# Kernel optimization log

Measured on AMD Instinct MI355X. Metric: run time of the kernel, lower is better.

## Reference

```python
import jax, jax.numpy as jnp
import numpy as np

N_NODES = 20000
N_EDGES = 320000
N_ADJ = 4
D = 256
CSTR = [0, 1]          # constrained adjacency subset for the last step
RATIO = 1.0
LN_EPS = 1e-5


def setup_inputs() -> dict:
    key = jax.random.key(0)
    ks = jax.random.split(key, 10)
    x = jax.random.normal(ks[0], (N_NODES, D), dtype=jnp.float32)
    rows = jax.random.randint(ks[1], (N_ADJ, N_EDGES), 0, N_NODES)
    cols = jax.random.randint(ks[2], (N_ADJ, N_EDGES), 0, N_NODES)
    vals = jax.random.uniform(ks[3], (N_ADJ, N_EDGES), dtype=jnp.float32)
    W = jax.random.normal(ks[4], (D, D), dtype=jnp.float32) * (1.0 / np.sqrt(D))
    b = jax.random.normal(ks[5], (D,), dtype=jnp.float32) * 0.02
    ws_seq_0 = jax.random.uniform(ks[6], (2, N_ADJ - 1), dtype=jnp.float32)
    ws_seq_1 = jax.random.uniform(ks[7], (len(CSTR),), dtype=jnp.float32)
    ws_res_0 = jax.random.uniform(ks[8], (1, N_ADJ), dtype=jnp.float32)
    ws_res_1 = jax.random.uniform(ks[9], (2, len(CSTR) + 1), dtype=jnp.float32)
    return {"x": x, "rows": rows, "cols": cols, "vals": vals, "W": W, "b": b,
            "ws_seq_0": ws_seq_0, "ws_seq_1": ws_seq_1,
            "ws_res_0": ws_res_0, "ws_res_1": ws_res_1}


def reference(x, rows, cols, vals, W, b, ws_seq_0, ws_seq_1, ws_res_0, ws_res_1):
    n_nodes = x.shape[0]

    def spmm(a, h):
        # sparse [n,n] @ h : gather source features, scale, scatter-add by row
        return jax.ops.segment_sum(vals[a][:, None] * h[cols[a]], rows[a],
                                   num_segments=n_nodes)

    def op(h, adj_ids, w):
        # Op with k=1: random.sample selects ALL operators -> weighted mean
        acc = w[0] * spmm(adj_ids[0], h)
        for j, a in enumerate(adj_ids[1:], start=1):
            acc = acc + w[j] * spmm(a, h)
        return acc / len(adj_ids)

    h = x @ W + b                      # affine: [n_nodes, D]
    states = [h]
    # step i=0: seq only (res sum over states[:0] is empty -> 0), edge == 1
    s1 = op(states[0], [0, 1, 2], ws_seq_0[0])          # adjs[:-1]
    states.append(s1)
    # step i=1: seq on states[1] over adjs[:-1], res on states[0] over all adjs
    s2 = op(states[1], [0, 1, 2], ws_seq_0[1]) + RATIO * op(states[0], [0, 1, 2, 3], ws_res_0[0])
    states.append(s2)
    # last step: cstr adjacencies for seq; cstr + last adj for residuals
    out_seq = op(states[2], CSTR, ws_seq_1)
    res_ids = CSTR + [N_ADJ - 1]
    out_res = op(states[0], res_ids, ws_res_1[0]) + op(states[1], res_ids, ws_res_1[1])
    out = out_seq + RATIO * out_res
    # LayerNorm without affine params
    mu = jnp.mean(out, axis=-1, keepdims=True)
    var = jnp.var(out, axis=-1, keepdims=True)
    out = (out - mu) * jax.lax.rsqrt(var + LN_EPS)
    return jax.nn.gelu(out, approximate=False)
```

## Files before the change

### kernel.cpp

```cpp
#include <hip/hip_runtime.h>
#include <hip/hip_bf16.h>

#define N_NODES 20000
#define N_EDGES 320000
#define N_ADJ   4
#define D       256
#define DH      128
#define RPA     20004

#define NBUCK   79
#define NGRP    40
#define EPB     8000
#define GCAP    192
#define NBSORT  (NBUCK * N_ADJ)
#define MMBLK   1250

typedef __attribute__((ext_vector_type(8))) short bf8;
typedef __attribute__((ext_vector_type(4))) float f4;


__device__ __forceinline__ unsigned f2bf_bits(float x) {
    unsigned u = __float_as_uint(x);
    return (u + 0x7FFFu + ((u >> 16) & 1u)) >> 16;
}
__device__ __forceinline__ unsigned pack_bf2(float lo, float hi) {
    return f2bf_bits(lo) | (f2bf_bits(hi) << 16);
}
__device__ __forceinline__ float bf_lo(unsigned p) { return __uint_as_float(p << 16); }
__device__ __forceinline__ float bf_hi(unsigned p) { return __uint_as_float(p & 0xFFFF0000u); }


__global__ __launch_bounds__(1024) void prep_kernel(const int* __restrict__ rows,
                                                    const int* __restrict__ cols,
                                                    const float* __restrict__ vals,
                                                    int* __restrict__ cnt,
                                                    uint2* __restrict__ stage,
                                                    const float* __restrict__ W,
                                                    uint4* __restrict__ wh,
                                                    uint4* __restrict__ wl) {
    __shared__ int lcnt[NBUCK];
    int g = blockIdx.x, a = blockIdx.y, t = threadIdx.x;

    if (g >= NGRP) {
        if (a != 0) return;
        for (int i = (g - NGRP) * 1024 + t; i < 8192; i += 2048) {
            int lane = i & 63;
            int tile = i >> 6;
            int ks = tile >> 4, n = tile & 15;
            int m = lane & 15, quad = lane >> 4;
            int col = n * 16 + m;
            int k0  = ks * 32 + quad * 8;
            unsigned hbits[8], lbits[8];
            #pragma unroll
            for (int j = 0; j < 8; ++j) {
                float v = W[(k0 + j) * D + col];
                unsigned hb = f2bf_bits(v);
                float lo = v - __uint_as_float(hb << 16);
                hbits[j] = hb;
                lbits[j] = f2bf_bits(lo);
            }
            uint4 hh, ll;
            hh.x = hbits[0] | (hbits[1] << 16); hh.y = hbits[2] | (hbits[3] << 16);
            hh.z = hbits[4] | (hbits[5] << 16); hh.w = hbits[6] | (hbits[7] << 16);
            ll.x = lbits[0] | (lbits[1] << 16); ll.y = lbits[2] | (lbits[3] << 16);
            ll.z = lbits[4] | (lbits[5] << 16); ll.w = lbits[6] | (lbits[7] << 16);
            wh[i] = hh;
            wl[i] = ll;
        }
        return;
    }

    if (t < NBUCK) lcnt[t] = 0;
    __syncthreads();
    int e0 = g * EPB;
    for (int i = 0; i < EPB; i += 1024) {
        int e = e0 + i + t;
        if (i + t < EPB) {
            int r   = rows[a * N_EDGES + e];
            int c   = cols[a * N_EDGES + e];
            float v = vals[a * N_EDGES + e];
            int b   = r >> 8;
            int idx = atomicAdd(&lcnt[b], 1);
            if (idx < GCAP) {
                stage[(size_t)((a * NBUCK + b) * NGRP + g) * GCAP + idx] =
                    make_uint2((f2bf_bits(v) << 16) | (unsigned)c, (unsigned)(r & 255));
            }
        }
    }
    __syncthreads();
    if (t < NBUCK) cnt[(a * NBUCK + t) * NGRP + g] = min(lcnt[t], GCAP);
}


__global__ __launch_bounds__(256) void bsmm_kernel(const float* __restrict__ x,
                                                   const uint4* __restrict__ wh,
                                                   const uint4* __restrict__ wl,
                                                   const float* __restrict__ bvec,
                                                   unsigned* __restrict__ hp,
                                                   const int* __restrict__ cnt,
                                                   const uint2* __restrict__ stage,
                                                   unsigned* __restrict__ csr,
                                                   int* __restrict__ row_ptr) {
    __shared__ int cbs[NGRP];
    __shared__ int scn[256];
    __shared__ int offs[256];
    __shared__ int gbase_s;
    int t = threadIdx.x;

    if (blockIdx.x >= NBSORT) {
        int wid = t >> 6, lane = t & 63;
        int r0 = (blockIdx.x - NBSORT) * 16;
        int m = lane & 15, quad = lane >> 4;

        const float* xr = x + (size_t)(r0 + m) * D + quad * 8;
        bf8 ah[8], al[8];
        #pragma unroll
        for (int ks = 0; ks < 8; ++ks) {
            float4 v0 = *(const float4*)(xr + ks * 32);
            float4 v1 = *(const float4*)(xr + ks * 32 + 4);
            float xs[8] = {v0.x, v0.y, v0.z, v0.w, v1.x, v1.y, v1.z, v1.w};
            #pragma unroll
            for (int j = 0; j < 8; ++j) {
                unsigned hb = f2bf_bits(xs[j]);
                float lo = xs[j] - __uint_as_float(hb << 16);
                ah[ks][j] = (short)hb;
                al[ks][j] = (short)f2bf_bits(lo);
            }
        }

        #pragma unroll
        for (int i = 0; i < 4; ++i) {
            int n = wid * 4 + i;
            f4 c = {0.f, 0.f, 0.f, 0.f};
            #pragma unroll
            for (int ks = 0; ks < 8; ++ks) {
                uint4 bh4 = wh[(ks * 16 + n) * 64 + lane];
                uint4 bl4 = wl[(ks * 16 + n) * 64 + lane];
                bf8 bh = *(bf8*)&bh4;
                bf8 bl = *(bf8*)&bl4;
                c = __builtin_amdgcn_mfma_f32_16x16x32_bf16(ah[ks], bh, c, 0, 0, 0);
                c = __builtin_amdgcn_mfma_f32_16x16x32_bf16(al[ks], bh, c, 0, 0, 0);
                c = __builtin_amdgcn_mfma_f32_16x16x32_bf16(ah[ks], bl, c, 0, 0, 0);
            }
            int col = n * 16 + m;
            float bb = bvec[col];
            #pragma unroll
            for (int reg = 0; reg < 4; ++reg) {
                float v = c[reg] + bb;
                float o = __shfl_xor(v, 1, 64);
                if ((m & 1) == 0) {
                    hp[(r0 + quad * 4 + reg) * DH + (col >> 1)] = pack_bf2(v, o);
                }
            }
        }
        return;
    }

    int linear = blockIdx.x;
    int a = linear / NBUCK, b = linear % NBUCK;

    if (t == 0) gbase_s = 0;
    scn[t] = 0;
    offs[t] = 0;
    if (t < NGRP) cbs[t] = cnt[(a * NBUCK + b) * NGRP + t];
    __syncthreads();

    int part = 0;
    for (int i = t; i < b * NGRP; i += 256) part += cnt[a * (NBUCK * NGRP) + i];
    #pragma unroll
    for (int off = 32; off > 0; off >>= 1) part += __shfl_xor(part, off, 64);
    if ((t & 63) == 0) atomicAdd(&gbase_s, part);

    const uint2* sb = stage + (size_t)(a * NBUCK + b) * NGRP * GCAP;

    for (int i = t; i < NGRP * GCAP; i += 256) {
        int g = i / GCAP, idx = i - g * GCAP;
        if (idx < cbs[g]) atomicAdd(&scn[sb[i].y], 1);
    }
    __syncthreads();

    int mycnt = scn[t];
    for (int off = 1; off < 256; off <<= 1) {
        int add = (t >= off) ? scn[t - off] : 0;
        __syncthreads();
        scn[t] += add;
        __syncthreads();
    }
    int excl = scn[t] - mycnt;
    __syncthreads();
    scn[t] = excl;
    __syncthreads();

    int gbase = gbase_s;
    for (int i = t; i < NGRP * GCAP; i += 256) {
        int g = i / GCAP, idx = i - g * GCAP;
        if (idx < cbs[g]) {
            uint2 rec = sb[i];
            int pos = scn[rec.y] + atomicAdd(&offs[rec.y], 1);
            csr[(size_t)a * N_EDGES + gbase + pos] = rec.x;
        }
    }
    int r = b * 256 + t;
    if (r <= N_NODES) row_ptr[(size_t)a * RPA + r] = gbase + excl;
}


__device__ __forceinline__ void gather_seg(const unsigned* __restrict__ E, int beg, int end,
                                           const uint2* __restrict__ feat2, int lane,
                                           float* __restrict__ s ) {
    int n = end - beg;
    const unsigned* e = E + beg;
    int m8 = n & ~7;
    if (m8) {
        unsigned rec[8];
        #pragma unroll
        for (int j = 0; j < 8; ++j) rec[j] = e[j];
        for (int i = 8; ; i += 8) {
            uint2 p[8];
            #pragma unroll
            for (int j = 0; j < 8; ++j)
                p[j] = feat2[((rec[j] & 0xFFFFu) << 6) + lane];
            bool more = i < m8;
            unsigned nrec[8];
            if (more) {
                #pragma unroll
                for (int j = 0; j < 8; ++j) nrec[j] = e[i + j];
            }
            #pragma unroll
            for (int j = 0; j < 8; ++j) {
                float v = __uint_as_float(rec[j] & 0xFFFF0000u);
                s[0] += v * bf_lo(p[j].x);
                s[1] += v * bf_hi(p[j].x);
                s[2] += v * bf_lo(p[j].y);
                s[3] += v * bf_hi(p[j].y);
            }
            if (!more) break;
            #pragma unroll
            for (int j = 0; j < 8; ++j) rec[j] = nrec[j];
        }
    }
    for (int i = m8; i < n; ++i) {
        unsigned rr = e[i];
        uint2 pp = feat2[((rr & 0xFFFFu) << 6) + lane];
        float vv = __uint_as_float(rr & 0xFFFF0000u);
        s[0] += vv * bf_lo(pp.x);
        s[1] += vv * bf_hi(pp.x);
        s[2] += vv * bf_lo(pp.y);
        s[3] += vv * bf_hi(pp.y);
    }
}


__global__ __launch_bounds__(256) void stage1_kernel(const uint2* __restrict__ hp2,
                                                     const int* __restrict__ row_ptr,
                                                     const unsigned* __restrict__ csr,
                                                     const float* __restrict__ wseq0,
                                                     const float* __restrict__ wres0,
                                                     const float* __restrict__ wres1,
                                                     uint2* __restrict__ s1p2,
                                                     uint2* __restrict__ s2p2,
                                                     float4* __restrict__ outp4) {
    int t = threadIdx.x, wid = t >> 6, lane = t & 63;
    int r = blockIdx.x * 4 + wid;
    float acc[N_ADJ][4];
    #pragma unroll
    for (int a = 0; a < N_ADJ; ++a) {
        acc[a][0] = acc[a][1] = acc[a][2] = acc[a][3] = 0.f;
        const int* rp = row_ptr + (size_t)a * RPA;
        int beg = __builtin_amdgcn_readfirstlane(rp[r]);
        int end = __builtin_amdgcn_readfirstlane(rp[r + 1]);
        gather_seg(csr + (size_t)a * N_EDGES, beg, end, hp2, lane, acc[a]);
    }
    const float third = 1.f / 3.f;
    float w0 = wseq0[0] * third, w1 = wseq0[1] * third, w2 = wseq0[2] * third;
    float q0 = wres0[0] * 0.25f, q1 = wres0[1] * 0.25f, q2 = wres0[2] * 0.25f, q3 = wres0[3] * 0.25f;
    float u0 = wres1[0] * third, u1 = wres1[1] * third, u2 = wres1[2] * third;
    float s1v[4], s2v[4], ov[4];
    #pragma unroll
    for (int j = 0; j < 4; ++j) {
        s1v[j] = w0 * acc[0][j] + w1 * acc[1][j] + w2 * acc[2][j];
        s2v[j] = q0 * acc[0][j] + q1 * acc[1][j] + q2 * acc[2][j] + q3 * acc[3][j];
        ov[j]  = u0 * acc[0][j] + u1 * acc[1][j] + u2 * acc[3][j];
    }
    int o = r * 64 + lane;
    s1p2[o]  = make_uint2(pack_bf2(s1v[0], s1v[1]), pack_bf2(s1v[2], s1v[3]));
    s2p2[o]  = make_uint2(pack_bf2(s2v[0], s2v[1]), pack_bf2(s2v[2], s2v[3]));
    outp4[o] = make_float4(ov[0], ov[1], ov[2], ov[3]);
}


__global__ __launch_bounds__(256) void stage2_kernel(const uint2* __restrict__ s1p2,
                                                     const int* __restrict__ row_ptr,
                                                     const unsigned* __restrict__ csr,
                                                     const float* __restrict__ wseq0,
                                                     const float* __restrict__ wres1,
                                                     uint2* __restrict__ s2p2,
                                                     float4* __restrict__ outp4) {
    int t = threadIdx.x, wid = t >> 6, lane = t & 63;
    int r = blockIdx.x * 4 + wid;
    float acc[N_ADJ][4];
    #pragma unroll
    for (int a = 0; a < N_ADJ; ++a) {
        acc[a][0] = acc[a][1] = acc[a][2] = acc[a][3] = 0.f;
        const int* rp = row_ptr + (size_t)a * RPA;
        int beg = __builtin_amdgcn_readfirstlane(rp[r]);
        int end = __builtin_amdgcn_readfirstlane(rp[r + 1]);
        gather_seg(csr + (size_t)a * N_EDGES, beg, end, s1p2, lane, acc[a]);
    }
    const float third = 1.f / 3.f;
    float w3 = wseq0[3] * third, w4 = wseq0[4] * third, w5 = wseq0[5] * third;
    float u3 = wres1[3] * third, u4 = wres1[4] * third, u5 = wres1[5] * third;
    int o = r * 64 + lane;
    uint2 sp = s2p2[o];
    float c0 = bf_lo(sp.x) + w3 * acc[0][0] + w4 * acc[1][0] + w5 * acc[2][0];
    float c1 = bf_hi(sp.x) + w3 * acc[0][1] + w4 * acc[1][1] + w5 * acc[2][1];
    float c2 = bf_lo(sp.y) + w3 * acc[0][2] + w4 * acc[1][2] + w5 * acc[2][2];
    float c3 = bf_hi(sp.y) + w3 * acc[0][3] + w4 * acc[1][3] + w5 * acc[2][3];
    s2p2[o] = make_uint2(pack_bf2(c0, c1), pack_bf2(c2, c3));
    float4 op = outp4[o];
    op.x += u3 * acc[0][0] + u4 * acc[1][0] + u5 * acc[3][0];
    op.y += u3 * acc[0][1] + u4 * acc[1][1] + u5 * acc[3][1];
    op.z += u3 * acc[0][2] + u4 * acc[1][2] + u5 * acc[3][2];
    op.w += u3 * acc[0][3] + u4 * acc[1][3] + u5 * acc[3][3];
    outp4[o] = op;
}


__global__ __launch_bounds__(256) void stage3_kernel(const uint2* __restrict__ s2p2,
                                                     const int* __restrict__ row_ptr,
                                                     const unsigned* __restrict__ csr,
                                                     const float* __restrict__ wseq1,
                                                     float4* __restrict__ outp4) {
    int t = threadIdx.x, wid = t >> 6, lane = t & 63;
    int r = blockIdx.x * 4 + wid;
    float acc[2][4];
    #pragma unroll
    for (int a = 0; a < 2; ++a) {
        acc[a][0] = acc[a][1] = acc[a][2] = acc[a][3] = 0.f;
        const int* rp = row_ptr + (size_t)a * RPA;
        int beg = __builtin_amdgcn_readfirstlane(rp[r]);
        int end = __builtin_amdgcn_readfirstlane(rp[r + 1]);
        gather_seg(csr + (size_t)a * N_EDGES, beg, end, s2p2, lane, acc[a]);
    }
    float e0 = wseq1[0] * 0.5f, e1 = wseq1[1] * 0.5f;
    int o = r * 64 + lane;
    float4 op = outp4[o];
    float v0 = op.x + e0 * acc[0][0] + e1 * acc[1][0];
    float v1 = op.y + e0 * acc[0][1] + e1 * acc[1][1];
    float v2 = op.z + e0 * acc[0][2] + e1 * acc[1][2];
    float v3 = op.w + e0 * acc[0][3] + e1 * acc[1][3];

    float sv = v0 + v1 + v2 + v3;
    float sq = v0 * v0 + v1 * v1 + v2 * v2 + v3 * v3;
    #pragma unroll
    for (int off = 32; off > 0; off >>= 1) {
        sv += __shfl_xor(sv, off, 64);
        sq += __shfl_xor(sq, off, 64);
    }
    float mu   = sv * (1.f / 256.f);
    float var  = sq * (1.f / 256.f) - mu * mu;
    float rstd = rsqrtf(var + 1e-5f);
    float y0 = (v0 - mu) * rstd;
    float y1 = (v1 - mu) * rstd;
    float y2 = (v2 - mu) * rstd;
    float y3 = (v3 - mu) * rstd;
    const float is2 = 0.70710678118654752440f;
    outp4[o] = make_float4(0.5f * y0 * (1.f + erff(y0 * is2)),
                           0.5f * y1 * (1.f + erff(y1 * is2)),
                           0.5f * y2 * (1.f + erff(y2 * is2)),
                           0.5f * y3 * (1.f + erff(y3 * is2)));
}


extern "C" void kernel_launch(void* const* d_in, const int* in_sizes, int n_in,
                              void* d_out, int out_size, void* d_ws, size_t ws_size,
                              hipStream_t stream) {
    const float* x     = (const float*)d_in[0];
    const int*   rows  = (const int*)d_in[1];
    const int*   cols  = (const int*)d_in[2];
    const float* vals  = (const float*)d_in[3];
    const float* W     = (const float*)d_in[4];
    const float* b     = (const float*)d_in[5];
    const float* wseq0 = (const float*)d_in[6];
    const float* wseq1 = (const float*)d_in[7];
    const float* wres0 = (const float*)d_in[8];
    const float* wres1 = (const float*)d_in[9];
    float4* outp4 = (float4*)d_out;

    char* p = (char*)d_ws;
    unsigned* hp  = (unsigned*)p; p += (size_t)N_NODES * DH * 4;
    unsigned* s1p = (unsigned*)p; p += (size_t)N_NODES * DH * 4;
    unsigned* s2p = (unsigned*)p; p += (size_t)N_NODES * DH * 4;
    int* row_ptr  = (int*)p;      p += (size_t)N_ADJ * RPA * 4;
    int* cnt      = (int*)p;      p += (N_ADJ * NBUCK * NGRP * 4 + 127) / 128 * 128;
    uint4* wh     = (uint4*)p;    p += 8192 * 16;
    uint4* wl     = (uint4*)p;    p += 8192 * 16;
    unsigned* csr = (unsigned*)p;
    uint2* stage  = (uint2*)s1p;

    prep_kernel<<<dim3(NGRP + 2, N_ADJ), 1024, 0, stream>>>(rows, cols, vals, cnt,
                                                            stage, W, wh, wl);
    bsmm_kernel<<<NBSORT + MMBLK, 256, 0, stream>>>(x, wh, wl, b, hp,
                                                    cnt, stage, csr, row_ptr);

    stage1_kernel<<<N_NODES / 4, 256, 0, stream>>>((const uint2*)hp, row_ptr, csr,
                                                   wseq0, wres0, wres1,
                                                   (uint2*)s1p, (uint2*)s2p, outp4);
    stage2_kernel<<<N_NODES / 4, 256, 0, stream>>>((const uint2*)s1p, row_ptr, csr,
                                                   wseq0, wres1, (uint2*)s2p, outp4);
    stage3_kernel<<<N_NODES / 4, 256, 0, stream>>>((const uint2*)s2p, row_ptr, csr,
                                                   wseq1, outp4);
}
```

Baseline: 310.8 us.

## Split stage kernels into row-chunk launches and halve sort group size

Each gather stage now runs as four launches covering 5000 rows each instead of one launch over all rows, with a row-base argument added to the stage kernels. Separately, the edge-bucketing prep uses twice as many groups with half as many edges per block and a smaller group capacity. The chunked launches may change cache locality or scheduling, but they add launch overhead and do not by themselves create cross-stage overlap on a single stream. The sort retuning trades more blocks and counters against less work per block.

Measured after the change: 364.6 us. 17.3% more time.

```diff
diff --git a/kernel.cpp b/kernel.cpp
--- a/kernel.cpp
+++ b/kernel.cpp
@@ -9,11 +9,12 @@
 #define RPA     20004
 
 #define NBUCK   79
-#define NGRP    40
-#define EPB     8000
-#define GCAP    192
+#define NGRP    80
+#define EPB     4000
+#define GCAP    100
 #define NBSORT  (NBUCK * N_ADJ)
 #define MMBLK   1250
+#define SGRID   1250
 
 typedef __attribute__((ext_vector_type(8))) short bf8;
 typedef __attribute__((ext_vector_type(4))) float f4;
@@ -259,9 +260,10 @@
                                                      const float* __restrict__ wres1,
                                                      uint2* __restrict__ s1p2,
                                                      uint2* __restrict__ s2p2,
-                                                     float4* __restrict__ outp4) {
+                                                     float4* __restrict__ outp4,
+                                                     int rbase) {
     int t = threadIdx.x, wid = t >> 6, lane = t & 63;
-    int r = blockIdx.x * 4 + wid;
+    int r = rbase + blockIdx.x * 4 + wid;
     float acc[N_ADJ][4];
     #pragma unroll
     for (int a = 0; a < N_ADJ; ++a) {
@@ -295,9 +297,10 @@
                                                      const float* __restrict__ wseq0,
                                                      const float* __restrict__ wres1,
                                                      uint2* __restrict__ s2p2,
-                                                     float4* __restrict__ outp4) {
+                                                     float4* __restrict__ outp4,
+                                                     int rbase) {
     int t = threadIdx.x, wid = t >> 6, lane = t & 63;
-    int r = blockIdx.x * 4 + wid;
+    int r = rbase + blockIdx.x * 4 + wid;
     float acc[N_ADJ][4];
     #pragma unroll
     for (int a = 0; a < N_ADJ; ++a) {
@@ -330,9 +333,10 @@
                                                      const int* __restrict__ row_ptr,
                                                      const unsigned* __restrict__ csr,
                                                      const float* __restrict__ wseq1,
-                                                     float4* __restrict__ outp4) {
+                                                     float4* __restrict__ outp4,
+                                                     int rbase) {
     int t = threadIdx.x, wid = t >> 6, lane = t & 63;
-    int r = blockIdx.x * 4 + wid;
+    int r = rbase + blockIdx.x * 4 + wid;
     float acc[2][4];
     #pragma unroll
     for (int a = 0; a < 2; ++a) {
@@ -392,7 +396,7 @@
     unsigned* s1p = (unsigned*)p; p += (size_t)N_NODES * DH * 4;
     unsigned* s2p = (unsigned*)p; p += (size_t)N_NODES * DH * 4;
     int* row_ptr  = (int*)p;      p += (size_t)N_ADJ * RPA * 4;
-    int* cnt      = (int*)p;      p += (N_ADJ * NBUCK * NGRP * 4 + 127) / 128 * 128;
+    int* cnt      = (int*)p;      p += ((size_t)N_ADJ * NBUCK * NGRP * 4 + 127) / 128 * 128;
     uint4* wh     = (uint4*)p;    p += 8192 * 16;
     uint4* wl     = (uint4*)p;    p += 8192 * 16;
     unsigned* csr = (unsigned*)p;
@@ -403,11 +407,16 @@
     bsmm_kernel<<<NBSORT + MMBLK, 256, 0, stream>>>(x, wh, wl, b, hp,
                                                     cnt, stage, csr, row_ptr);
 
-    stage1_kernel<<<N_NODES / 4, 256, 0, stream>>>((const uint2*)hp, row_ptr, csr,
-                                                   wseq0, wres0, wres1,
-                                                   (uint2*)s1p, (uint2*)s2p, outp4);
-    stage2_kernel<<<N_NODES / 4, 256, 0, stream>>>((const uint2*)s1p, row_ptr, csr,
-                                                   wseq0, wres1, (uint2*)s2p, outp4);
-    stage3_kernel<<<N_NODES / 4, 256, 0, stream>>>((const uint2*)s2p, row_ptr, csr,
-                                                   wseq1, outp4);
-}
+    for (int q = 0; q < 4; ++q)
+        stage1_kernel<<<SGRID, 256, 0, stream>>>((const uint2*)hp, row_ptr, csr,
+                                                 wseq0, wres0, wres1,
+                                                 (uint2*)s1p, (uint2*)s2p, outp4,
+                                                 q * 5000);
+    for (int q = 0; q < 4; ++q)
+        stage2_kernel<<<SGRID, 256, 0, stream>>>((const uint2*)s1p, row_ptr, csr,
+                                                 wseq0, wres1, (uint2*)s2p, outp4,
+                                                 q * 5000);
+    for (int q = 0; q < 4; ++q)
+        stage3_kernel<<<SGRID, 256, 0, stream>>>((const uint2*)s2p, row_ptr, csr,
+                                                 wseq1, outp4, q * 5000);
+}
```

## Split fused sort/matmul kernel and double edge-group count for bucketing

Applied to the files above, without the earlier changes.

Splits the combined bucket-sort plus affine-matmul kernel into two launches: a sort kernel with 1024 threads per block and a separate MFMA matmul kernel. It also doubles the number of edge groups in the prep stage, which halves edges per group and shrinks the per-group capacity. The aim is more parallelism in the prep and sort phases and wider blocks for the scatter loops. The cost is losing the overlap between sort and matmul blocks inside one launch, plus one extra launch. The tighter per-group capacity also leaves less headroom before bucket overflow.

Result: slower. 320.6 us (+3.1%).

```diff
diff --git a/kernel.cpp b/kernel.cpp
--- a/kernel.cpp
+++ b/kernel.cpp
@@ -9,9 +9,9 @@
 #define RPA     20004
 
 #define NBUCK   79
-#define NGRP    40
-#define EPB     8000
-#define GCAP    192
+#define NGRP    80
+#define EPB     4000
+#define GCAP    100
 #define NBSORT  (NBUCK * N_ADJ)
 #define MMBLK   1250
 
@@ -92,107 +92,50 @@
 }
 
 
-__global__ __launch_bounds__(256) void bsmm_kernel(const float* __restrict__ x,
-                                                   const uint4* __restrict__ wh,
-                                                   const uint4* __restrict__ wl,
-                                                   const float* __restrict__ bvec,
-                                                   unsigned* __restrict__ hp,
-                                                   const int* __restrict__ cnt,
-                                                   const uint2* __restrict__ stage,
-                                                   unsigned* __restrict__ csr,
-                                                   int* __restrict__ row_ptr) {
+__global__ __launch_bounds__(1024) void bsort_kernel(const int* __restrict__ cnt,
+                                                     const uint2* __restrict__ stage,
+                                                     unsigned* __restrict__ csr,
+                                                     int* __restrict__ row_ptr) {
     __shared__ int cbs[NGRP];
     __shared__ int scn[256];
     __shared__ int offs[256];
     __shared__ int gbase_s;
     int t = threadIdx.x;
-
-    if (blockIdx.x >= NBSORT) {
-        int wid = t >> 6, lane = t & 63;
-        int r0 = (blockIdx.x - NBSORT) * 16;
-        int m = lane & 15, quad = lane >> 4;
-
-        const float* xr = x + (size_t)(r0 + m) * D + quad * 8;
-        bf8 ah[8], al[8];
-        #pragma unroll
-        for (int ks = 0; ks < 8; ++ks) {
-            float4 v0 = *(const float4*)(xr + ks * 32);
-            float4 v1 = *(const float4*)(xr + ks * 32 + 4);
-            float xs[8] = {v0.x, v0.y, v0.z, v0.w, v1.x, v1.y, v1.z, v1.w};
-            #pragma unroll
-            for (int j = 0; j < 8; ++j) {
-                unsigned hb = f2bf_bits(xs[j]);
-                float lo = xs[j] - __uint_as_float(hb << 16);
-                ah[ks][j] = (short)hb;
-                al[ks][j] = (short)f2bf_bits(lo);
-            }
-        }
-
-        #pragma unroll
-        for (int i = 0; i < 4; ++i) {
-            int n = wid * 4 + i;
-            f4 c = {0.f, 0.f, 0.f, 0.f};
-            #pragma unroll
-            for (int ks = 0; ks < 8; ++ks) {
-                uint4 bh4 = wh[(ks * 16 + n) * 64 + lane];
-                uint4 bl4 = wl[(ks * 16 + n) * 64 + lane];
-                bf8 bh = *(bf8*)&bh4;
-                bf8 bl = *(bf8*)&bl4;
-                c = __builtin_amdgcn_mfma_f32_16x16x32_bf16(ah[ks], bh, c, 0, 0, 0);
-                c = __builtin_amdgcn_mfma_f32_16x16x32_bf16(al[ks], bh, c, 0, 0, 0);
-                c = __builtin_amdgcn_mfma_f32_16x16x32_bf16(ah[ks], bl, c, 0, 0, 0);
-            }
-            int col = n * 16 + m;
-            float bb = bvec[col];
-            #pragma unroll
-            for (int reg = 0; reg < 4; ++reg) {
-                float v = c[reg] + bb;
-                float o = __shfl_xor(v, 1, 64);
-                if ((m & 1) == 0) {
-                    hp[(r0 + quad * 4 + reg) * DH + (col >> 1)] = pack_bf2(v, o);
-                }
-            }
-        }
-        return;
-    }
-
-    int linear = blockIdx.x;
-    int a = linear / NBUCK, b = linear % NBUCK;
+    int a = blockIdx.x / NBUCK, b = blockIdx.x % NBUCK;
 
     if (t == 0) gbase_s = 0;
-    scn[t] = 0;
-    offs[t] = 0;
+    if (t < 256) { scn[t] = 0; offs[t] = 0; }
     if (t < NGRP) cbs[t] = cnt[(a * NBUCK + b) * NGRP + t];
     __syncthreads();
 
     int part = 0;
-    for (int i = t; i < b * NGRP; i += 256) part += cnt[a * (NBUCK * NGRP) + i];
+    for (int i = t; i < b * NGRP; i += 1024) part += cnt[a * (NBUCK * NGRP) + i];
     #pragma unroll
     for (int off = 32; off > 0; off >>= 1) part += __shfl_xor(part, off, 64);
     if ((t & 63) == 0) atomicAdd(&gbase_s, part);
 
     const uint2* sb = stage + (size_t)(a * NBUCK + b) * NGRP * GCAP;
 
-    for (int i = t; i < NGRP * GCAP; i += 256) {
+    for (int i = t; i < NGRP * GCAP; i += 1024) {
         int g = i / GCAP, idx = i - g * GCAP;
         if (idx < cbs[g]) atomicAdd(&scn[sb[i].y], 1);
     }
     __syncthreads();
 
-    int mycnt = scn[t];
+    int mycnt = (t < 256) ? scn[t] : 0;
     for (int off = 1; off < 256; off <<= 1) {
-        int add = (t >= off) ? scn[t - off] : 0;
+        int add = (t >= off && t < 256) ? scn[t - off] : 0;
         __syncthreads();
-        scn[t] += add;
+        if (t < 256) scn[t] += add;
         __syncthreads();
     }
-    int excl = scn[t] - mycnt;
-    __syncthreads();
-    scn[t] = excl;
+    int excl = (t < 256) ? scn[t] - mycnt : 0;
+    __syncthreads();
+    if (t < 256) scn[t] = excl;
     __syncthreads();
 
     int gbase = gbase_s;
-    for (int i = t; i < NGRP * GCAP; i += 256) {
+    for (int i = t; i < NGRP * GCAP; i += 1024) {
         int g = i / GCAP, idx = i - g * GCAP;
         if (idx < cbs[g]) {
             uint2 rec = sb[i];
@@ -201,7 +144,61 @@
         }
     }
     int r = b * 256 + t;
-    if (r <= N_NODES) row_ptr[(size_t)a * RPA + r] = gbase + excl;
+    if (t < 256 && r <= N_NODES) row_ptr[(size_t)a * RPA + r] = gbase + excl;
+}
+
+
+__global__ __launch_bounds__(256) void mm_kernel(const float* __restrict__ x,
+                                                 const uint4* __restrict__ wh,
+                                                 const uint4* __restrict__ wl,
+                                                 const float* __restrict__ bvec,
+                                                 unsigned* __restrict__ hp) {
+    int t = threadIdx.x;
+    int wid = t >> 6, lane = t & 63;
+    int r0 = blockIdx.x * 16;
+    int m = lane & 15, quad = lane >> 4;
+
+    const float* xr = x + (size_t)(r0 + m) * D + quad * 8;
+    bf8 ah[8], al[8];
+    #pragma unroll
+    for (int ks = 0; ks < 8; ++ks) {
+        float4 v0 = *(const float4*)(xr + ks * 32);
+        float4 v1 = *(const float4*)(xr + ks * 32 + 4);
+        float xs[8] = {v0.x, v0.y, v0.z, v0.w, v1.x, v1.y, v1.z, v1.w};
+        #pragma unroll
+        for (int j = 0; j < 8; ++j) {
+            unsigned hb = f2bf_bits(xs[j]);
+            float lo = xs[j] - __uint_as_float(hb << 16);
+            ah[ks][j] = (short)hb;
+            al[ks][j] = (short)f2bf_bits(lo);
+        }
+    }
+
+    #pragma unroll
+    for (int i = 0; i < 4; ++i) {
+        int n = wid * 4 + i;
+        f4 c = {0.f, 0.f, 0.f, 0.f};
+        #pragma unroll
+        for (int ks = 0; ks < 8; ++ks) {
+            uint4 bh4 = wh[(ks * 16 + n) * 64 + lane];
+            uint4 bl4 = wl[(ks * 16 + n) * 64 + lane];
+            bf8 bh = *(bf8*)&bh4;
+            bf8 bl = *(bf8*)&bl4;
+            c = __builtin_amdgcn_mfma_f32_16x16x32_bf16(ah[ks], bh, c, 0, 0, 0);
+            c = __builtin_amdgcn_mfma_f32_16x16x32_bf16(al[ks], bh, c, 0, 0, 0);
+            c = __builtin_amdgcn_mfma_f32_16x16x32_bf16(ah[ks], bl, c, 0, 0, 0);
+        }
+        int col = n * 16 + m;
+        float bb = bvec[col];
+        #pragma unroll
+        for (int reg = 0; reg < 4; ++reg) {
+            float v = c[reg] + bb;
+            float o = __shfl_xor(v, 1, 64);
+            if ((m & 1) == 0) {
+                hp[(r0 + quad * 4 + reg) * DH + (col >> 1)] = pack_bf2(v, o);
+            }
+        }
+    }
 }
 
 
@@ -392,7 +389,7 @@
     unsigned* s1p = (unsigned*)p; p += (size_t)N_NODES * DH * 4;
     unsigned* s2p = (unsigned*)p; p += (size_t)N_NODES * DH * 4;
     int* row_ptr  = (int*)p;      p += (size_t)N_ADJ * RPA * 4;
-    int* cnt      = (int*)p;      p += (N_ADJ * NBUCK * NGRP * 4 + 127) / 128 * 128;
+    int* cnt      = (int*)p;      p += ((size_t)N_ADJ * NBUCK * NGRP * 4 + 127) / 128 * 128;
     uint4* wh     = (uint4*)p;    p += 8192 * 16;
     uint4* wl     = (uint4*)p;    p += 8192 * 16;
     unsigned* csr = (unsigned*)p;
@@ -400,8 +397,8 @@
 
     prep_kernel<<<dim3(NGRP + 2, N_ADJ), 1024, 0, stream>>>(rows, cols, vals, cnt,
                                                             stage, W, wh, wl);
-    bsmm_kernel<<<NBSORT + MMBLK, 256, 0, stream>>>(x, wh, wl, b, hp,
-                                                    cnt, stage, csr, row_ptr);
+    bsort_kernel<<<NBSORT, 1024, 0, stream>>>(cnt, stage, csr, row_ptr);
+    mm_kernel<<<MMBLK, 256, 0, stream>>>(x, wh, wl, b, hp);
 
     stage1_kernel<<<N_NODES / 4, 256, 0, stream>>>((const uint2*)hp, row_ptr, csr,
                                                    wseq0, wres0, wres1,
```
